# Kernel optimization log

Measured on AMD Instinct MI355X. Metric: run time of the kernel, lower is better.

The kernel has to match this reference:

```python
import jax, jax.numpy as jnp
import numpy as np

B, N, C, O, K, D = 32, 2048, 64, 64, 3, 16

def setup_inputs() -> dict:
    key = jax.random.key(0)
    ks = jax.random.split(key, 6)
    x = jax.random.normal(ks[0], (B, N, C), dtype=jnp.float32)
    node_embeddings = jax.random.normal(ks[1], (N, D), dtype=jnp.float32)
    adj_m = jax.random.uniform(ks[2], (N, N), dtype=jnp.float32)
    weights_pool = jax.random.normal(ks[3], (D, K, C, O), dtype=jnp.float32) * 0.1
    bias_pool = jax.random.normal(ks[4], (D, O), dtype=jnp.float32) * 0.1
    sa_weight = jax.random.normal(ks[5], (N, 2 * N), dtype=jnp.float32) * (1.0 / np.sqrt(2 * N))
    return {"x": x, "node_embeddings": node_embeddings, "adj_m": adj_m,
            "weights_pool": weights_pool, "bias_pool": bias_pool, "sa_weight": sa_weight}

def reference(x, node_embeddings, adj_m, weights_pool, bias_pool, sa_weight):
    n = node_embeddings.shape[0]
    # learned adaptive adjacency [N,N]
    supports = jax.nn.softmax(jax.nn.relu(node_embeddings @ node_embeddings.T), axis=1)
    # SpatialAttention: 1x1 conv over 2N channels == matmul with [N,2N] weight
    z = jnp.concatenate([supports, adj_m], axis=1) @ sa_weight.T  # [N,N]
    s2 = jax.nn.sigmoid(z)
    supports = s2 * adj_m + (1.0 - s2) * supports
    # Chebyshev polynomial basis
    support_set = [jnp.eye(n, dtype=supports.dtype), supports]
    for _ in range(2, K):
        support_set.append(2.0 * supports @ support_set[-1] - support_set[-2])
    supports_k = jnp.stack(support_set, axis=0)  # [K,N,N]
    # per-node generated weights/bias from embeddings
    weights = jnp.einsum('nd,dkio->nkio', node_embeddings, weights_pool)  # [N,K,C,O]
    bias = node_embeddings @ bias_pool  # [N,O]
    # graph conv: aggregate then per-node matmul
    x_g = jnp.einsum('knm,bmc->bnkc', supports_k, x)  # [B,N,K,C]
    x_gconv = jnp.einsum('bnki,nkio->bno', x_g, weights) + bias  # [B,N,O]
    return x_gconv
```

## Files before the change

### kernel.cpp

```cpp
#include <hip/hip_runtime.h>


typedef unsigned short u16;
typedef float f32x4 __attribute__((ext_vector_type(4)));
typedef __bf16 bf16x8 __attribute__((ext_vector_type(8)));
typedef unsigned short u16x8 __attribute__((ext_vector_type(8)));

#define PSTRIDE ((size_t)2048 * 2048)

__device__ __forceinline__ u16 f2bf(float f) {
    unsigned u = __float_as_uint(f);
    u += 0x7FFFu + ((u >> 16) & 1u);
    return (u16)(u >> 16);
}
__device__ __forceinline__ float bf2f(u16 h) {
    return __uint_as_float((unsigned)h << 16);
}
__device__ __forceinline__ void gl_lds16(const void* g, void* l) {
    __builtin_amdgcn_global_load_lds(
        (const __attribute__((address_space(1))) unsigned*)g,
        (__attribute__((address_space(3))) unsigned*)l, 16, 0, 0);
}

__global__ __launch_bounds__(256)
void preamble(const float* __restrict__ E, const float* __restrict__ adj,
              const float* __restrict__ saw, const float* __restrict__ x,
              const float* __restrict__ Wp, const float* __restrict__ bp,
              float* __restrict__ zf, u16* __restrict__ Acat,
              u16* __restrict__ sawb, u16* __restrict__ xtT,
              u16* __restrict__ Wpb, float* __restrict__ Wpbf,
              float* __restrict__ bias, u16* __restrict__ xn, int mode) {
    __shared__ u16 t[64][65];
    __shared__ float Bp[1024];
    const int bid = blockIdx.x, tid = threadIdx.x;

    if (bid < 256) {
        const int c0 = (bid & 31) * 64, r0 = (bid >> 5) * 256;
        const int r = r0 + tid;
        const float4* Er = (const float4*)(E + (size_t)r * 16);
        float4 e0 = Er[0], e1 = Er[1], e2 = Er[2], e3 = Er[3];
        *(float4*)(Bp + tid * 4) = *(const float4*)(E + (size_t)c0 * 16 + tid * 4);
        __syncthreads();
        float* zr = zf + (size_t)r * 2048 + c0;
#pragma unroll
        for (int cc = 0; cc < 4; ++cc) {
            float acc[16];
#pragma unroll
            for (int c = 0; c < 16; ++c) {
                const float* bp2 = Bp + (cc * 16 + c) * 16;
                float s = 0.f;
                s = fmaf(e0.x, bp2[0], s);  s = fmaf(e0.y, bp2[1], s);
                s = fmaf(e0.z, bp2[2], s);  s = fmaf(e0.w, bp2[3], s);
                s = fmaf(e1.x, bp2[4], s);  s = fmaf(e1.y, bp2[5], s);
                s = fmaf(e1.z, bp2[6], s);  s = fmaf(e1.w, bp2[7], s);
                s = fmaf(e2.x, bp2[8], s);  s = fmaf(e2.y, bp2[9], s);
                s = fmaf(e2.z, bp2[10], s); s = fmaf(e2.w, bp2[11], s);
                s = fmaf(e3.x, bp2[12], s); s = fmaf(e3.y, bp2[13], s);
                s = fmaf(e3.z, bp2[14], s); s = fmaf(e3.w, bp2[15], s);
                acc[c] = fmaxf(s, 0.f);
            }
#pragma unroll
            for (int q = 0; q < 4; ++q)
                *(float4*)(zr + cc * 16 + q * 4) =
                    make_float4(acc[q * 4], acc[q * 4 + 1], acc[q * 4 + 2], acc[q * 4 + 3]);
        }
    } else if (bid < 1792) {
        const size_t NADJ = 1048576, STRIDE = (size_t)1536 * 256;
        const size_t e0 = (size_t)(bid - 256) * 256 + tid;
        float4 v[8];
#pragma unroll
        for (int it = 0; it < 8; ++it) {
            size_t idx = e0 + (size_t)it * STRIDE;
            const float* src = (idx < NADJ) ? (adj + idx * 4) : (saw + (idx - NADJ) * 4);
            v[it] = *(const float4*)src;
        }
#pragma unroll
        for (int it = 0; it < 8; ++it) {
            size_t idx = e0 + (size_t)it * STRIDE;
            ushort4 o = make_ushort4(f2bf(v[it].x), f2bf(v[it].y), f2bf(v[it].z), f2bf(v[it].w));
            if (idx < NADJ) {
                size_t j = idx * 4;
                int n = (int)(j >> 11), c = (int)(j & 2047);
                *(ushort4*)(Acat + (size_t)n * 4096 + 2048 + c) = o;
            } else {
                *(ushort4*)(sawb + (idx - NADJ) * 4) = o;
            }
        }
    } else if (bid < 2816) {
        int local = bid - 1792;
        int m0 = (local & 31) * 64, b = local >> 5;
        int c = tid & 63, g = tid >> 6;
#pragma unroll
        for (int r = 0; r < 16; ++r) {
            int mm = g * 16 + r;
            t[mm][c] = f2bf(x[((size_t)b * 2048 + m0 + mm) * 64 + c]);
        }
        __syncthreads();
#pragma unroll
        for (int r = 0; r < 16; ++r) {
            int cc = g * 16 + r;
            xtT[((size_t)b * 64 + cc) * 2048 + m0 + c] = t[c][cc];
        }
        if (mode) {
#pragma unroll
            for (int r = 0; r < 16; ++r) {
                int mm = g * 16 + r;
                xn[((size_t)(m0 + mm)) * 2048 + b * 64 + c] = t[mm][c];
            }
        }
    } else {
        int local = bid - 2816;
        if (local < 16) {
            const int d = local;
            const float* base = Wp + (size_t)d * 12288;
            for (int idx = tid; idx < 12288; idx += 256) {
                int o = idx / 192, ki = idx - o * 192;
                int k = ki >> 6, i = ki & 63;
                float v;
                if (k == 0)      v = base[i * 64 + o] - base[2 * 4096 + i * 64 + o];
                else if (k == 1) v = base[4096 + i * 64 + o];
                else             v = 2.f * base[2 * 4096 + i * 64 + o];
                size_t dst = (size_t)(d * 64 + o) * 192 + ki;
                Wpb[dst] = f2bf(v);
                Wpbf[dst] = v;
            }
        } else {
            const int nb = local - 16;
#pragma unroll
            for (int it = 0; it < 8; ++it) {
                int idx = tid + it * 256;
                int n = nb * 32 + (idx >> 6), o = idx & 63;
                float s = 0.f;
#pragma unroll
                for (int d = 0; d < 16; ++d) s = fmaf(E[n * 16 + d], bp[d * 64 + o], s);
                bias[(size_t)n * 64 + o] = s;
            }
        }
    }
}

__global__ __launch_bounds__(256)
void mid(const float* __restrict__ zf, u16* __restrict__ Acat,
         const float* __restrict__ E, const float* __restrict__ Wpbf,
         u16* __restrict__ Wnb) {
    __shared__ float red[4];
    __shared__ float Es[32 * 16];
    const int bid = blockIdx.x, tid = threadIdx.x;
    if (bid < 2048) {
        const int n = bid, lane = tid & 63, wave = tid >> 6;
        const float* zr = zf + (size_t)n * 2048;
        float4 a = *(const float4*)(zr + tid * 8);
        float4 b = *(const float4*)(zr + tid * 8 + 4);
        float mx = fmaxf(fmaxf(fmaxf(a.x, a.y), fmaxf(a.z, a.w)),
                         fmaxf(fmaxf(b.x, b.y), fmaxf(b.z, b.w)));
        for (int off = 32; off; off >>= 1) mx = fmaxf(mx, __shfl_down(mx, off, 64));
        if (lane == 0) red[wave] = mx;
        __syncthreads();
        mx = fmaxf(fmaxf(red[0], red[1]), fmaxf(red[2], red[3]));
        __syncthreads();
        float v[8] = {__expf(a.x - mx), __expf(a.y - mx), __expf(a.z - mx), __expf(a.w - mx),
                      __expf(b.x - mx), __expf(b.y - mx), __expf(b.z - mx), __expf(b.w - mx)};
        float sum = v[0] + v[1] + v[2] + v[3] + v[4] + v[5] + v[6] + v[7];
        for (int off = 32; off; off >>= 1) sum += __shfl_down(sum, off, 64);
        if (lane == 0) red[wave] = sum;
        __syncthreads();
        sum = red[0] + red[1] + red[2] + red[3];
        float inv = 1.f / sum;
        u16* orow = Acat + (size_t)n * 4096 + tid * 8;
        *(ushort4*)orow = make_ushort4(f2bf(v[0] * inv), f2bf(v[1] * inv),
                                       f2bf(v[2] * inv), f2bf(v[3] * inv));
        *(ushort4*)(orow + 4) = make_ushort4(f2bf(v[4] * inv), f2bf(v[5] * inv),
                                             f2bf(v[6] * inv), f2bf(v[7] * inv));
    } else {
        const int w = bid - 2048;
        const int c0 = (w % 12) * 1024, n0 = (w / 12) * 32;
        for (int j = tid; j < 512; j += 256) Es[j] = E[(size_t)n0 * 16 + j];
        float4 wf[16];
#pragma unroll
        for (int d = 0; d < 16; ++d)
            wf[d] = *(const float4*)(Wpbf + (size_t)d * 12288 + c0 + tid * 4);
        __syncthreads();
        for (int nl = 0; nl < 32; ++nl) {
            float4 s = make_float4(0.f, 0.f, 0.f, 0.f);
#pragma unroll
            for (int d = 0; d < 16; ++d) {
                float e = Es[nl * 16 + d];
                s.x = fmaf(e, wf[d].x, s.x);
                s.y = fmaf(e, wf[d].y, s.y);
                s.z = fmaf(e, wf[d].z, s.z);
                s.w = fmaf(e, wf[d].w, s.w);
            }
            *(ushort4*)(Wnb + (size_t)(n0 + nl) * 12288 + c0 + tid * 4) =
                make_ushort4(f2bf(s.x), f2bf(s.y), f2bf(s.z), f2bf(s.w));
        }
    }
}

__global__ __launch_bounds__(512, 2)
void gemm_bt256(const u16* __restrict__ A, const u16* __restrict__ Bt,
                u16* __restrict__ Cp, int M, int N, int K, int Kh) {
    __shared__ alignas(16) u16 As[2][256 * 64];
    __shared__ alignas(16) u16 Bs[2][256 * 64];
    const int tid = threadIdx.x, lane = tid & 63, wave = tid >> 6;

    const int nbx = gridDim.x, nby = gridDim.y, nbz = gridDim.z;
    const int nwg = nbx * nby * nbz;
    int lin = (blockIdx.z * nby + blockIdx.y) * nbx + blockIdx.x;
    if ((nwg & 7) == 0) lin = (lin & 7) * (nwg >> 3) + (lin >> 3);
    const int bz = lin / (nbx * nby);
    const int r2 = lin - bz * nbx * nby;
    const int by = r2 / nbx, bx = r2 - by * nbx;

    const int m0 = by * 256, n0 = bx * 256;
    const int kbeg = bz * Kh;
    const int NT = Kh >> 6;
    const int wm = (wave >> 2) * 128, wn = (wave & 3) * 64;
    const int ml = lane & 15, c0l = lane >> 4;

    int sI[4], rowI[4], gcI[4];
#pragma unroll
    for (int r = 0; r < 4; ++r) {
        int s = r * 512 + tid;
        sI[r] = s; rowI[r] = s >> 3; gcI[r] = (s & 7) ^ ((s >> 3) & 7);
    }

    f32x4 acc[8][4] = {};
    bf16x8 af[4][2], bv[2][2];

#define LOADA(r_, kt_, buf_) \
    gl_lds16(A + (size_t)(m0 + rowI[r_]) * K + (kt_) + gcI[r_] * 8, \
             &As[buf_][sI[r_] * 8])
#define LOADB(r_, kt_, buf_) \
    gl_lds16(Bt + (size_t)(n0 + rowI[r_]) * K + (kt_) + gcI[r_] * 8, \
             &Bs[buf_][sI[r_] * 8])

#define DSRA(qa_) \
    _Pragma("unroll") \
    for (int i = 0; i < 4; ++i) { \
        const int mr = wm + (qa_) * 64 + i * 16 + ml; \
        _Pragma("unroll") \
        for (int ks = 0; ks < 2; ++ks) \
            af[i][ks] = *(const bf16x8*)(Asc + mr * 64 + (((c0l + ks * 4) ^ (mr & 7)) * 8)); \
    }
#define DSRB(qb_) \
    _Pragma("unroll") \
    for (int j = 0; j < 2; ++j) { \
        const int nr = wn + (qb_) * 32 + j * 16 + ml; \
        _Pragma("unroll") \
        for (int ks = 0; ks < 2; ++ks) \
            bv[j][ks] = *(const bf16x8*)(Bsc + nr * 64 + (((c0l + ks * 4) ^ (nr & 7)) * 8)); \
    }
#define MMQ(io_, jo_) \
    __builtin_amdgcn_s_barrier(); \
    asm volatile("s_waitcnt lgkmcnt(0)" ::: "memory"); \
    __builtin_amdgcn_s_setprio(1); \
    _Pragma("unroll") \
    for (int ks = 0; ks < 2; ++ks) \
        _Pragma("unroll") \
        for (int i = 0; i < 4; ++i) \
            _Pragma("unroll") \
            for (int j = 0; j < 2; ++j) \
                acc[(io_) + i][(jo_) + j] = __builtin_amdgcn_mfma_f32_16x16x32_bf16( \
                    af[i][ks], bv[j][ks], acc[(io_) + i][(jo_) + j], 0, 0, 0); \
    __builtin_amdgcn_s_setprio(0);

#pragma unroll
    for (int r = 0; r < 4; ++r) LOADA(r, kbeg, 0);
#pragma unroll
    for (int r = 0; r < 4; ++r) LOADB(r, kbeg, 0);
    asm volatile("s_waitcnt vmcnt(0)" ::: "memory");
    __builtin_amdgcn_s_barrier();

    for (int t = 0; t < NT - 1; ++t) {
        const int cur = t & 1, nxt = cur ^ 1;
        const u16* Asc = As[cur];
        const u16* Bsc = Bs[cur];
        const int k1 = kbeg + (t + 1) * 64;

        DSRA(0); DSRB(0);
        LOADB(0, k1, nxt); LOADB(1, k1, nxt);
        MMQ(0, 0);
        __builtin_amdgcn_s_barrier();

        DSRB(1);
        LOADB(2, k1, nxt); LOADB(3, k1, nxt);
        MMQ(0, 2);
        asm volatile("s_waitcnt vmcnt(4)" ::: "memory");
        __builtin_amdgcn_s_barrier();

        DSRA(1);
        LOADA(0, k1, nxt); LOADA(2, k1, nxt);
        MMQ(4, 2);
        __builtin_amdgcn_s_barrier();

        DSRB(0);
        LOADA(1, k1, nxt); LOADA(3, k1, nxt);
        MMQ(4, 0);
        asm volatile("s_waitcnt vmcnt(2)" ::: "memory");
        __builtin_amdgcn_s_barrier();
    }

    {
        const int cur = (NT - 1) & 1;
        const u16* Asc = As[cur];
        const u16* Bsc = Bs[cur];

        DSRA(0); DSRB(0);
        MMQ(0, 0);
        __builtin_amdgcn_s_barrier();

        DSRB(1);
        MMQ(0, 2);
        asm volatile("s_waitcnt vmcnt(0)" ::: "memory");
        __builtin_amdgcn_s_barrier();

        DSRA(1);
        MMQ(4, 2);
        __builtin_amdgcn_s_barrier();

        DSRB(0);
        MMQ(4, 0);
    }

#undef LOADA
#undef LOADB
#undef DSRA
#undef DSRB
#undef MMQ

    const int col_l = lane & 15, rl = (lane >> 4) * 4;
    u16* Cz = Cp + (size_t)bz * M * N;
#pragma unroll
    for (int i = 0; i < 8; ++i)
#pragma unroll
        for (int j = 0; j < 4; ++j)
#pragma unroll
            for (int r = 0; r < 4; ++r) {
                int row = m0 + wm + i * 16 + rl + r;
                int col = n0 + wn + j * 16 + col_l;
                Cz[(size_t)row * N + col] = f2bf(acc[i][j][r]);
            }
}

__global__ __launch_bounds__(256)
void reduce_z(const u16* __restrict__ p, const u16* __restrict__ Acat,
              u16* __restrict__ S) {
    const size_t base = ((size_t)blockIdx.x * 256 + threadIdx.x) * 4;
    const size_t STRIDE = (size_t)1024 * 256 * 4;
#pragma unroll
    for (int it = 0; it < 4; ++it) {
        size_t j = base + (size_t)it * STRIDE;
        ushort4 p0 = *(const ushort4*)(p + j);
        ushort4 p1 = *(const ushort4*)(p + PSTRIDE + j);
        ushort4 p2 = *(const ushort4*)(p + 2 * PSTRIDE + j);
        ushort4 p3 = *(const ushort4*)(p + 3 * PSTRIDE + j);
        int row = (int)(j >> 11), col = (int)(j & 2047);
        ushort4 sp = *(const ushort4*)(Acat + (size_t)row * 4096 + col);
        ushort4 ad = *(const ushort4*)(Acat + (size_t)row * 4096 + 2048 + col);
        float z0 = bf2f(p0.x) + bf2f(p1.x) + bf2f(p2.x) + bf2f(p3.x);
        float z1 = bf2f(p0.y) + bf2f(p1.y) + bf2f(p2.y) + bf2f(p3.y);
        float z2 = bf2f(p0.z) + bf2f(p1.z) + bf2f(p2.z) + bf2f(p3.z);
        float z3 = bf2f(p0.w) + bf2f(p1.w) + bf2f(p2.w) + bf2f(p3.w);
        float s0 = 1.f / (1.f + __expf(-z0)), s1 = 1.f / (1.f + __expf(-z1));
        float s2 = 1.f / (1.f + __expf(-z2)), s3 = 1.f / (1.f + __expf(-z3));
        ushort4 o = make_ushort4(
            f2bf(s0 * bf2f(ad.x) + (1.f - s0) * bf2f(sp.x)),
            f2bf(s1 * bf2f(ad.y) + (1.f - s1) * bf2f(sp.y)),
            f2bf(s2 * bf2f(ad.z) + (1.f - s2) * bf2f(sp.z)),
            f2bf(s3 * bf2f(ad.w) + (1.f - s3) * bf2f(sp.w)));
        *(ushort4*)(S + j) = o;
    }
}

__global__ __launch_bounds__(256)
void reduceT(const u16* __restrict__ p, u16* __restrict__ xg1o,
             u16* __restrict__ xg1T, int mode) {
    __shared__ u16 t[64][68];
    int bx = blockIdx.x * 64, by = blockIdx.y * 64;
    int cg = threadIdx.x & 15, rg = threadIdx.x >> 4;
    int b = bx >> 6;
#pragma unroll
    for (int rr = 0; rr < 4; ++rr) {
        int row = rg * 4 + rr;
        size_t idx = (size_t)(by + row) * 2048 + bx + cg * 4;
        ushort4 q0 = *(const ushort4*)(p + idx);
        ushort4 q1 = *(const ushort4*)(p + PSTRIDE + idx);
        ushort4 q2 = *(const ushort4*)(p + 2 * PSTRIDE + idx);
        ushort4 q3 = *(const ushort4*)(p + 3 * PSTRIDE + idx);
        ushort4 v = make_ushort4(
            f2bf(bf2f(q0.x) + bf2f(q1.x) + bf2f(q2.x) + bf2f(q3.x)),
            f2bf(bf2f(q0.y) + bf2f(q1.y) + bf2f(q2.y) + bf2f(q3.y)),
            f2bf(bf2f(q0.z) + bf2f(q1.z) + bf2f(q2.z) + bf2f(q3.z)),
            f2bf(bf2f(q0.w) + bf2f(q1.w) + bf2f(q2.w) + bf2f(q3.w)));
        if (mode) *(ushort4*)(xg1o + idx) = v;
        else      *(ushort4*)(xg1o + ((size_t)b * 2048 + by + row) * 64 + cg * 4) = v;
        *(ushort4*)(&t[row][cg * 4]) = v;
    }
    __syncthreads();
    int c = threadIdx.x & 63, g = threadIdx.x >> 6;
#pragma unroll
    for (int r = 0; r < 16; ++r) {
        int row = g * 16 + r;
        xg1T[(size_t)(bx + row) * 2048 + by + c] = t[c][row];
    }
}

__global__ __launch_bounds__(256, 4)
void gconv_wn(const u16* __restrict__ xn, const u16* __restrict__ xg1n,
              const u16* __restrict__ p, const u16* __restrict__ Wnb,
              const float* __restrict__ bias, float* __restrict__ out) {
    __shared__ alignas(16) u16 As[32 * 192];
    __shared__ alignas(16) u16 Bs[64 * 192];
    const int n = blockIdx.x, tid = threadIdx.x;
    const int lane = tid & 63, wave = tid >> 6;
    const int wn2 = wave * 16;
    const int ml = lane & 15, c0l = lane >> 4;
    const int col = lane & 15, rl = (lane >> 4) * 4;

#pragma unroll
    for (int it = 0; it < 6; ++it) {
        int s = tid + it * 256;
        int row = s / 24, sc = s - row * 24;
        int gc = (sc & 24) | ((sc ^ row) & 7);
        gl_lds16(Wnb + (size_t)n * 12288 + (size_t)row * 192 + gc * 8, Bs + (size_t)s * 8);
    }
#pragma unroll
    for (int it = 0; it < 3; ++it) {
        int s = tid + it * 256;
        int row = s / 24, sc = s - row * 24;
        int gc = (sc & 24) | ((sc ^ row) & 7);
        u16x8 v;
        if (gc < 8) {
            v = *(const u16x8*)(xn + (size_t)n * 2048 + row * 64 + (gc & 7) * 8);
        } else if (gc < 16) {
            v = *(const u16x8*)(xg1n + (size_t)n * 2048 + row * 64 + (gc & 7) * 8);
        } else {
            const u16* pp = p + (size_t)n * 2048 + row * 64 + (gc & 7) * 8;
            u16x8 q0 = *(const u16x8*)pp;
            u16x8 q1 = *(const u16x8*)(pp + PSTRIDE);
            u16x8 q2 = *(const u16x8*)(pp + 2 * PSTRIDE);
            u16x8 q3 = *(const u16x8*)(pp + 3 * PSTRIDE);
#pragma unroll
            for (int tt = 0; tt < 8; ++tt)
                v[tt] = f2bf(bf2f(q0[tt]) + bf2f(q1[tt]) + bf2f(q2[tt]) + bf2f(q3[tt]));
        }
        *(u16x8*)(As + (size_t)s * 8) = v;
    }
    float bv0 = bias[(size_t)n * 64 + wn2 + col];
    f32x4 acc[2];
#pragma unroll
    for (int mt = 0; mt < 2; ++mt)
#pragma unroll
        for (int r = 0; r < 4; ++r) acc[mt][r] = bv0;
    __syncthreads();

#pragma unroll
    for (int ks = 0; ks < 6; ++ks) {
        int c = c0l + ks * 4;
        int o = wn2 + ml;
        bf16x8 bfrag = *(const bf16x8*)(Bs + (o * 24 + ((c & 24) | ((c ^ (o & 7)) & 7))) * 8);
#pragma unroll
        for (int mt = 0; mt < 2; ++mt) {
            int m = mt * 16 + ml;
            bf16x8 afrag = *(const bf16x8*)(As + (m * 24 + ((c & 24) | ((c ^ (m & 7)) & 7))) * 8);
            acc[mt] = __builtin_amdgcn_mfma_f32_16x16x32_bf16(afrag, bfrag, acc[mt], 0, 0, 0);
        }
    }
#pragma unroll
    for (int mt = 0; mt < 2; ++mt)
#pragma unroll
        for (int r = 0; r < 4; ++r) {
            int b = mt * 16 + rl + r;
            out[((size_t)b * 2048 + n) * 64 + wn2 + col] = acc[mt][r];
        }
}

__global__ __launch_bounds__(256, 2)
void gconv_mfma(const float* __restrict__ x, const u16* __restrict__ xg1,
                const u16* __restrict__ p, const u16* __restrict__ Wpb,
                const float* __restrict__ bias, const float* __restrict__ E,
                float* __restrict__ out) {
    __shared__ alignas(16) float El[16 * 128];
    const int tid = threadIdx.x, lane = tid & 63, wave = tid >> 6;
    const int m0 = blockIdx.x * 128, nb = m0 & 2047, bB = m0 >> 11;
    const int wm = (wave >> 1) * 64, wn = (wave & 1) * 32;
    const int ml = lane & 15, c0l = lane >> 4;
    const int col_l = lane & 15, rl = (lane >> 4) * 4;

#pragma unroll
    for (int it = 0; it < 8; ++it) {
        int idx = tid + it * 256;
        El[idx] = E[(size_t)(nb + (idx & 127)) * 16 + (idx >> 7)];
    }
    __syncthreads();

    bf16x8 af[4][6];
#pragma unroll
    for (int i = 0; i < 4; ++i) {
        const int row = m0 + wm + i * 16 + ml;
        const int n = row & 2047;
#pragma unroll
        for (int ks = 0; ks < 2; ++ks) {
            const float* xp = x + (size_t)row * 64 + (c0l + ks * 4) * 8;
            float4 a = *(const float4*)xp, b4 = *(const float4*)(xp + 4);
            u16x8 v;
            v[0] = f2bf(a.x);  v[1] = f2bf(a.y);  v[2] = f2bf(a.z);  v[3] = f2bf(a.w);
            v[4] = f2bf(b4.x); v[5] = f2bf(b4.y); v[6] = f2bf(b4.z); v[7] = f2bf(b4.w);
            af[i][ks] = __builtin_bit_cast(bf16x8, v);
        }
#pragma unroll
        for (int ks = 2; ks < 4; ++ks)
            af[i][ks] = *(const bf16x8*)(xg1 + (size_t)row * 64 + (c0l + ks * 4 - 8) * 8);
#pragma unroll
        for (int ks = 4; ks < 6; ++ks) {
            const u16* pp = p + (size_t)n * 2048 + bB * 64 + (c0l + ks * 4 - 16) * 8;
            u16x8 q0 = *(const u16x8*)pp;
            u16x8 q1 = *(const u16x8*)(pp + PSTRIDE);
            u16x8 q2 = *(const u16x8*)(pp + 2 * PSTRIDE);
            u16x8 q3 = *(const u16x8*)(pp + 3 * PSTRIDE);
            u16x8 v;
#pragma unroll
            for (int tt = 0; tt < 8; ++tt)
                v[tt] = f2bf(bf2f(q0[tt]) + bf2f(q1[tt]) + bf2f(q2[tt]) + bf2f(q3[tt]));
            af[i][ks] = __builtin_bit_cast(bf16x8, v);
        }
    }

    f32x4 oacc[4][2];
#pragma unroll
    for (int i = 0; i < 4; ++i)
#pragma unroll
        for (int j = 0; j < 2; ++j)
#pragma unroll
            for (int r = 0; r < 4; ++r)
                oacc[i][j][r] = bias[(size_t)(nb + wm + i * 16 + rl + r) * 64 + wn + j * 16 + col_l];

#pragma unroll 2
    for (int d = 0; d < 16; ++d) {
        bf16x8 bv[2][6];
#pragma unroll
        for (int j = 0; j < 2; ++j) {
            const u16* wp = Wpb + (size_t)(d * 64 + wn + j * 16 + ml) * 192 + c0l * 8;
#pragma unroll
            for (int ks = 0; ks < 6; ++ks)
                bv[j][ks] = *(const bf16x8*)(wp + ks * 32);
        }
        f32x4 tmp[4][2] = {};
#pragma unroll
        for (int ks = 0; ks < 6; ++ks)
#pragma unroll
            for (int i = 0; i < 4; ++i)
#pragma unroll
                for (int j = 0; j < 2; ++j)
                    tmp[i][j] = __builtin_amdgcn_mfma_f32_16x16x32_bf16(af[i][ks], bv[j][ks], tmp[i][j], 0, 0, 0);
#pragma unroll
        for (int i = 0; i < 4; ++i) {
            f32x4 ev = *(const f32x4*)(El + d * 128 + wm + i * 16 + rl);
#pragma unroll
            for (int r = 0; r < 4; ++r)
#pragma unroll
                for (int j = 0; j < 2; ++j)
                    oacc[i][j][r] = fmaf(ev[r], tmp[i][j][r], oacc[i][j][r]);
        }
    }
#pragma unroll
    for (int i = 0; i < 4; ++i)
#pragma unroll
        for (int j = 0; j < 2; ++j)
#pragma unroll
            for (int r = 0; r < 4; ++r)
                out[(size_t)(m0 + wm + i * 16 + rl + r) * 64 + wn + j * 16 + col_l] = oacc[i][j][r];
}

extern "C" void kernel_launch(void* const* d_in, const int* in_sizes, int n_in,
                              void* d_out, int out_size, void* d_ws, size_t ws_size,
                              hipStream_t stream) {
    const float* x   = (const float*)d_in[0];
    const float* E   = (const float*)d_in[1];
    const float* adj = (const float*)d_in[2];
    const float* Wp  = (const float*)d_in[3];
    const float* bp  = (const float*)d_in[4];
    const float* saw = (const float*)d_in[5];
    float* out = (float*)d_out;

    char* ws = (char*)d_ws;
    const size_t MB = 1u << 20;
    const int wn_mode = (ws_size >= 140 * MB) ? 1 : 0;

    u16*   Acat  = (u16*)(ws);
    u16*   sawb  = (u16*)(ws + 16 * MB);
    u16*   XtT   = (u16*)(ws + 32 * MB);
    u16*   Wpb   = (u16*)(ws + 40 * MB);
    float* bias  = (float*)(ws + 41 * MB);
    float* Wpbf  = (float*)(ws + 42 * MB);
    float* zf    = (float*)(ws + 48 * MB);
    u16*   part  = (u16*)(ws + 48 * MB);
    u16*   S_bf  = (u16*)(ws + 16 * MB);
    u16*   xg1T  = (u16*)(ws + 24 * MB);
    u16*   xg1o  = (u16*)(ws);
    u16*   xn    = (u16*)(ws + 80 * MB);
    u16*   Wnb   = (u16*)(ws + 88 * MB);

    preamble<<<2896, 256, 0, stream>>>(E, adj, saw, x, Wp, bp, zf, Acat, sawb, XtT,
                                       Wpb, Wpbf, bias, xn, wn_mode);
    mid<<<wn_mode ? 2816 : 2048, 256, 0, stream>>>(zf, Acat, E, Wpbf, Wnb);

    gemm_bt256<<<dim3(8, 8, 4), 512, 0, stream>>>(Acat, sawb, part, 2048, 2048, 4096, 1024);
    reduce_z<<<1024, 256, 0, stream>>>(part, Acat, S_bf);
    gemm_bt256<<<dim3(8, 8, 4), 512, 0, stream>>>(S_bf, XtT, part, 2048, 2048, 2048, 512);
    reduceT<<<dim3(32, 32), 256, 0, stream>>>(part, xg1o, xg1T, wn_mode);
    gemm_bt256<<<dim3(8, 8, 4), 512, 0, stream>>>(S_bf, xg1T, part, 2048, 2048, 2048, 512);

    if (wn_mode)
        gconv_wn<<<2048, 256, 0, stream>>>(xn, xg1o, part, Wnb, bias, out);
    else
        gconv_mfma<<<512, 256, 0, stream>>>(x, xg1o, part, Wpb, bias, E, out);
}
```

Baseline: 271.4 us.

## Fuse embedding product, ReLU and row softmax into one kernel, drop fp32 scratch

Adds a zsm kernel that loads all node embeddings into LDS (128KB), computes eight rows of relu(E·Eᵀ) per block in registers, and applies the row softmax before writing bf16 into Acat. This removes the 16MB fp32 zf round trip and the separate softmax pass in mid. The mid kernel now only generates per-node weights and is launched only in wn_mode. The cost is that zsm runs 256 blocks with a large LDS footprint, so occupancy is low, and it adds one more kernel launch before the preamble.

```diff
diff --git a/kernel.cpp b/kernel.cpp
--- a/kernel.cpp
+++ b/kernel.cpp
@@ -23,50 +23,101 @@
 }
 
 __global__ __launch_bounds__(256)
+void zsm(const float* __restrict__ E, u16* __restrict__ Acat) {
+    __shared__ float Et[16 * 2048];
+    __shared__ float redm[4][8], reds[4][8];
+    const int tid = threadIdx.x;
+    const int r0 = blockIdx.x * 8;
+
+#pragma unroll
+    for (int k = 0; k < 8; ++k) {
+        const int n = tid + 256 * k;
+        const float4* Er = (const float4*)(E + (size_t)n * 16);
+        float4 e0 = Er[0], e1 = Er[1], e2 = Er[2], e3 = Er[3];
+        Et[0 * 2048 + n] = e0.x;  Et[1 * 2048 + n] = e0.y;
+        Et[2 * 2048 + n] = e0.z;  Et[3 * 2048 + n] = e0.w;
+        Et[4 * 2048 + n] = e1.x;  Et[5 * 2048 + n] = e1.y;
+        Et[6 * 2048 + n] = e1.z;  Et[7 * 2048 + n] = e1.w;
+        Et[8 * 2048 + n] = e2.x;  Et[9 * 2048 + n] = e2.y;
+        Et[10 * 2048 + n] = e2.z; Et[11 * 2048 + n] = e2.w;
+        Et[12 * 2048 + n] = e3.x; Et[13 * 2048 + n] = e3.y;
+        Et[14 * 2048 + n] = e3.z; Et[15 * 2048 + n] = e3.w;
+    }
+    __syncthreads();
+
+    float z[8][8] = {};
+#pragma unroll
+    for (int d = 0; d < 16; ++d) {
+        const float* row = Et + d * 2048;
+        float ev[8];
+#pragma unroll
+        for (int k = 0; k < 8; ++k) ev[k] = row[tid + 256 * k];
+#pragma unroll
+        for (int r = 0; r < 8; ++r) {
+            float e = row[r0 + r];
+#pragma unroll
+            for (int k = 0; k < 8; ++k) z[r][k] = fmaf(e, ev[k], z[r][k]);
+        }
+    }
+    float mr[8];
+#pragma unroll
+    for (int r = 0; r < 8; ++r) {
+        float m = 0.f;
+#pragma unroll
+        for (int k = 0; k < 8; ++k) { z[r][k] = fmaxf(z[r][k], 0.f); m = fmaxf(m, z[r][k]); }
+        mr[r] = m;
+    }
+#pragma unroll
+    for (int off = 32; off; off >>= 1)
+#pragma unroll
+        for (int r = 0; r < 8; ++r) mr[r] = fmaxf(mr[r], __shfl_xor(mr[r], off, 64));
+    if ((tid & 63) == 0) {
+#pragma unroll
+        for (int r = 0; r < 8; ++r) redm[tid >> 6][r] = mr[r];
+    }
+    __syncthreads();
+#pragma unroll
+    for (int r = 0; r < 8; ++r)
+        mr[r] = fmaxf(fmaxf(redm[0][r], redm[1][r]), fmaxf(redm[2][r], redm[3][r]));
+    float sr[8];
+#pragma unroll
+    for (int r = 0; r < 8; ++r) {
+        float s = 0.f;
+#pragma unroll
+        for (int k = 0; k < 8; ++k) { z[r][k] = __expf(z[r][k] - mr[r]); s += z[r][k]; }
+        sr[r] = s;
+    }
+#pragma unroll
+    for (int off = 32; off; off >>= 1)
+#pragma unroll
+        for (int r = 0; r < 8; ++r) sr[r] += __shfl_xor(sr[r], off, 64);
+    if ((tid & 63) == 0) {
+#pragma unroll
+        for (int r = 0; r < 8; ++r) reds[tid >> 6][r] = sr[r];
+    }
+    __syncthreads();
+#pragma unroll
+    for (int r = 0; r < 8; ++r) {
+        float inv = 1.f / (reds[0][r] + reds[1][r] + reds[2][r] + reds[3][r]);
+        u16* orow = Acat + (size_t)(r0 + r) * 4096;
+#pragma unroll
+        for (int k = 0; k < 8; ++k) orow[tid + 256 * k] = f2bf(z[r][k] * inv);
+    }
+}
+
+__global__ __launch_bounds__(256)
 void preamble(const float* __restrict__ E, const float* __restrict__ adj,
               const float* __restrict__ saw, const float* __restrict__ x,
               const float* __restrict__ Wp, const float* __restrict__ bp,
-              float* __restrict__ zf, u16* __restrict__ Acat,
-              u16* __restrict__ sawb, u16* __restrict__ xtT,
+              u16* __restrict__ Acat, u16* __restrict__ sawb, u16* __restrict__ xtT,
               u16* __restrict__ Wpb, float* __restrict__ Wpbf,
               float* __restrict__ bias, u16* __restrict__ xn, int mode) {
     __shared__ u16 t[64][65];
-    __shared__ float Bp[1024];
     const int bid = blockIdx.x, tid = threadIdx.x;
 
-    if (bid < 256) {
-        const int c0 = (bid & 31) * 64, r0 = (bid >> 5) * 256;
-        const int r = r0 + tid;
-        const float4* Er = (const float4*)(E + (size_t)r * 16);
-        float4 e0 = Er[0], e1 = Er[1], e2 = Er[2], e3 = Er[3];
-        *(float4*)(Bp + tid * 4) = *(const float4*)(E + (size_t)c0 * 16 + tid * 4);
-        __syncthreads();
-        float* zr = zf + (size_t)r * 2048 + c0;
-#pragma unroll
-        for (int cc = 0; cc < 4; ++cc) {
-            float acc[16];
-#pragma unroll
-            for (int c = 0; c < 16; ++c) {
-                const float* bp2 = Bp + (cc * 16 + c) * 16;
-                float s = 0.f;
-                s = fmaf(e0.x, bp2[0], s);  s = fmaf(e0.y, bp2[1], s);
-                s = fmaf(e0.z, bp2[2], s);  s = fmaf(e0.w, bp2[3], s);
-                s = fmaf(e1.x, bp2[4], s);  s = fmaf(e1.y, bp2[5], s);
-                s = fmaf(e1.z, bp2[6], s);  s = fmaf(e1.w, bp2[7], s);
-                s = fmaf(e2.x, bp2[8], s);  s = fmaf(e2.y, bp2[9], s);
-                s = fmaf(e2.z, bp2[10], s); s = fmaf(e2.w, bp2[11], s);
-                s = fmaf(e3.x, bp2[12], s); s = fmaf(e3.y, bp2[13], s);
-                s = fmaf(e3.z, bp2[14], s); s = fmaf(e3.w, bp2[15], s);
-                acc[c] = fmaxf(s, 0.f);
-            }
-#pragma unroll
-            for (int q = 0; q < 4; ++q)
-                *(float4*)(zr + cc * 16 + q * 4) =
-                    make_float4(acc[q * 4], acc[q * 4 + 1], acc[q * 4 + 2], acc[q * 4 + 3]);
-        }
-    } else if (bid < 1792) {
+    if (bid < 1536) {
         const size_t NADJ = 1048576, STRIDE = (size_t)1536 * 256;
-        const size_t e0 = (size_t)(bid - 256) * 256 + tid;
+        const size_t e0 = (size_t)bid * 256 + tid;
         float4 v[8];
 #pragma unroll
         for (int it = 0; it < 8; ++it) {
@@ -86,8 +137,8 @@
                 *(ushort4*)(sawb + (idx - NADJ) * 4) = o;
             }
         }
-    } else if (bid < 2816) {
-        int local = bid - 1792;
+    } else if (bid < 2560) {
+        int local = bid - 1536;
         int m0 = (local & 31) * 64, b = local >> 5;
         int c = tid & 63, g = tid >> 6;
 #pragma unroll
@@ -109,7 +160,7 @@
             }
         }
     } else {
-        int local = bid - 2816;
+        int local = bid - 2560;
         if (local < 16) {
             const int d = local;
             const float* base = Wp + (size_t)d * 12288;
@@ -140,59 +191,29 @@
 }
 
 __global__ __launch_bounds__(256)
-void mid(const float* __restrict__ zf, u16* __restrict__ Acat,
-         const float* __restrict__ E, const float* __restrict__ Wpbf,
+void mid(const float* __restrict__ E, const float* __restrict__ Wpbf,
          u16* __restrict__ Wnb) {
-    __shared__ float red[4];
     __shared__ float Es[32 * 16];
-    const int bid = blockIdx.x, tid = threadIdx.x;
-    if (bid < 2048) {
-        const int n = bid, lane = tid & 63, wave = tid >> 6;
-        const float* zr = zf + (size_t)n * 2048;
-        float4 a = *(const float4*)(zr + tid * 8);
-        float4 b = *(const float4*)(zr + tid * 8 + 4);
-        float mx = fmaxf(fmaxf(fmaxf(a.x, a.y), fmaxf(a.z, a.w)),
-                         fmaxf(fmaxf(b.x, b.y), fmaxf(b.z, b.w)));
-        for (int off = 32; off; off >>= 1) mx = fmaxf(mx, __shfl_down(mx, off, 64));
-        if (lane == 0) red[wave] = mx;
-        __syncthreads();
-        mx = fmaxf(fmaxf(red[0], red[1]), fmaxf(red[2], red[3]));
-        __syncthreads();
-        float v[8] = {__expf(a.x - mx), __expf(a.y - mx), __expf(a.z - mx), __expf(a.w - mx),
-                      __expf(b.x - mx), __expf(b.y - mx), __expf(b.z - mx), __expf(b.w - mx)};
-        float sum = v[0] + v[1] + v[2] + v[3] + v[4] + v[5] + v[6] + v[7];
-        for (int off = 32; off; off >>= 1) sum += __shfl_down(sum, off, 64);
-        if (lane == 0) red[wave] = sum;
-        __syncthreads();
-        sum = red[0] + red[1] + red[2] + red[3];
-        float inv = 1.f / sum;
-        u16* orow = Acat + (size_t)n * 4096 + tid * 8;
-        *(ushort4*)orow = make_ushort4(f2bf(v[0] * inv), f2bf(v[1] * inv),
-                                       f2bf(v[2] * inv), f2bf(v[3] * inv));
-        *(ushort4*)(orow + 4) = make_ushort4(f2bf(v[4] * inv), f2bf(v[5] * inv),
-                                             f2bf(v[6] * inv), f2bf(v[7] * inv));
-    } else {
-        const int w = bid - 2048;
-        const int c0 = (w % 12) * 1024, n0 = (w / 12) * 32;
-        for (int j = tid; j < 512; j += 256) Es[j] = E[(size_t)n0 * 16 + j];
-        float4 wf[16];
-#pragma unroll
-        for (int d = 0; d < 16; ++d)
-            wf[d] = *(const float4*)(Wpbf + (size_t)d * 12288 + c0 + tid * 4);
-        __syncthreads();
-        for (int nl = 0; nl < 32; ++nl) {
-            float4 s = make_float4(0.f, 0.f, 0.f, 0.f);
-#pragma unroll
-            for (int d = 0; d < 16; ++d) {
-                float e = Es[nl * 16 + d];
-                s.x = fmaf(e, wf[d].x, s.x);
-                s.y = fmaf(e, wf[d].y, s.y);
-                s.z = fmaf(e, wf[d].z, s.z);
-                s.w = fmaf(e, wf[d].w, s.w);
-            }
-            *(ushort4*)(Wnb + (size_t)(n0 + nl) * 12288 + c0 + tid * 4) =
-                make_ushort4(f2bf(s.x), f2bf(s.y), f2bf(s.z), f2bf(s.w));
-        }
+    const int w = blockIdx.x, tid = threadIdx.x;
+    const int c0 = (w % 12) * 1024, n0 = (w / 12) * 32;
+    for (int j = tid; j < 512; j += 256) Es[j] = E[(size_t)n0 * 16 + j];
+    float4 wf[16];
+#pragma unroll
+    for (int d = 0; d < 16; ++d)
+        wf[d] = *(const float4*)(Wpbf + (size_t)d * 12288 + c0 + tid * 4);
+    __syncthreads();
+    for (int nl = 0; nl < 32; ++nl) {
+        float4 s = make_float4(0.f, 0.f, 0.f, 0.f);
+#pragma unroll
+        for (int d = 0; d < 16; ++d) {
+            float e = Es[nl * 16 + d];
+            s.x = fmaf(e, wf[d].x, s.x);
+            s.y = fmaf(e, wf[d].y, s.y);
+            s.z = fmaf(e, wf[d].z, s.z);
+            s.w = fmaf(e, wf[d].w, s.w);
+        }
+        *(ushort4*)(Wnb + (size_t)(n0 + nl) * 12288 + c0 + tid * 4) =
+            make_ushort4(f2bf(s.x), f2bf(s.y), f2bf(s.z), f2bf(s.w));
     }
 }
 
@@ -593,7 +614,6 @@
     u16*   Wpb   = (u16*)(ws + 40 * MB);
     float* bias  = (float*)(ws + 41 * MB);
     float* Wpbf  = (float*)(ws + 42 * MB);
-    float* zf    = (float*)(ws + 48 * MB);
     u16*   part  = (u16*)(ws + 48 * MB);
     u16*   S_bf  = (u16*)(ws + 16 * MB);
     u16*   xg1T  = (u16*)(ws + 24 * MB);
@@ -601,9 +621,11 @@
     u16*   xn    = (u16*)(ws + 80 * MB);
     u16*   Wnb   = (u16*)(ws + 88 * MB);
 
-    preamble<<<2896, 256, 0, stream>>>(E, adj, saw, x, Wp, bp, zf, Acat, sawb, XtT,
+    zsm<<<256, 256, 0, stream>>>(E, Acat);
+    preamble<<<2640, 256, 0, stream>>>(E, adj, saw, x, Wp, bp, Acat, sawb, XtT,
                                        Wpb, Wpbf, bias, xn, wn_mode);
-    mid<<<wn_mode ? 2816 : 2048, 256, 0, stream>>>(zf, Acat, E, Wpbf, Wnb);
+    if (wn_mode)
+        mid<<<768, 256, 0, stream>>>(E, Wpbf, Wnb);
 
     gemm_bt256<<<dim3(8, 8, 4), 512, 0, stream>>>(Acat, sawb, part, 2048, 2048, 4096, 1024);
     reduce_z<<<1024, 256, 0, stream>>>(part, Acat, S_bf);
```

After: 276.4 us. About the same (+1.8%).
